# Optimization experiments

Hardware: AMD Instinct MI355X
Metric: run time of the kernel (lower is better)

Reference implementation:

```python
import jax, jax.numpy as jnp
import numpy as np

N, K, C, H = 8192, 32, 192, 6
HD = C // H                       # head dim = 32
SCALE = HD ** -0.5
POS_BND = int(0.8 * K)            # 25 (OctFormer RPE: 0.8*patch_size*dilation**0.5, dilation=1)
RPE_NUM = 2 * POS_BND + 1         # 51
HID = 4 * C                       # mlp hidden


def setup_inputs() -> dict:
    key = jax.random.key(0)
    ks = jax.random.split(key, 18)
    w = lambda k, sh: (jax.random.normal(k, sh, jnp.float32) * 0.02)
    data = jax.random.normal(ks[0], (N, K, C), jnp.float32)
    # rel_pos: integer xyz offsets between points in a window, roughly in [-32, 32)
    rel_pos = jax.random.randint(ks[1], (N, K, K, 3), 0, 64, jnp.int32) - 32
    mask = jnp.where(jax.random.uniform(ks[2], (N, K, K)) < 0.05, -1e9, 0.0).astype(jnp.float32)
    return {
        "data": data,
        "mask": mask,
        "rel_pos": rel_pos,
        "ln1_g": jnp.ones((C,), jnp.float32),
        "ln1_b": jnp.zeros((C,), jnp.float32),
        "qkv_w": w(ks[3], (C, 3 * C)),
        "qkv_b": jnp.zeros((3 * C,), jnp.float32),
        "rpe_table": w(ks[4], (3 * RPE_NUM, H)),
        "proj_w": w(ks[5], (C, C)),
        "proj_b": jnp.zeros((C,), jnp.float32),
        "ln2_g": jnp.ones((C,), jnp.float32),
        "ln2_b": jnp.zeros((C,), jnp.float32),
        "mlp_w1": w(ks[6], (C, HID)),
        "mlp_b1": jnp.zeros((HID,), jnp.float32),
        "mlp_w2": w(ks[7], (HID, C)),
        "mlp_b2": jnp.zeros((C,), jnp.float32),
    }


def _layernorm(x, g, b):
    m = x.mean(-1, keepdims=True)
    v = ((x - m) ** 2).mean(-1, keepdims=True)
    return (x - m) * jax.lax.rsqrt(v + 1e-5) * g + b


def reference(data, mask, rel_pos, ln1_g, ln1_b, qkv_w, qkv_b, rpe_table,
              proj_w, proj_b, ln2_g, ln2_b, mlp_w1, mlp_b1, mlp_w2, mlp_b2):
    # --- windowed attention (OctreeAttention) ---
    x = _layernorm(data, ln1_g, ln1_b)                      # (N,K,C)
    qkv = (x @ qkv_w + qkv_b).reshape(N, K, 3, H, HD)
    qkv = qkv.transpose(2, 0, 3, 1, 4)                      # (3,N,H,K,HD)
    q, k, v = qkv[0] * SCALE, qkv[1], qkv[2]
    attn = jnp.einsum('nhqd,nhkd->nhqk', q, k)              # (N,H,K,K)
    # RPE: clamp xyz offsets, index per-axis rows of the table, sum over xyz
    idx = jnp.clip(rel_pos, -POS_BND, POS_BND) + POS_BND + jnp.arange(3, dtype=rel_pos.dtype) * RPE_NUM
    rpe = rpe_table[idx].sum(axis=3)                        # (N,K,K,H)
    attn = attn + rpe.transpose(0, 3, 1, 2) + mask[:, None, :, :]
    attn = jax.nn.softmax(attn, axis=-1)
    out = jnp.einsum('nhqk,nhkd->nqhd', attn, v).reshape(N, K, C)
    out = out @ proj_w + proj_b
    data = data + out                                       # residual (gamma1=1, drop_path=0)
    # --- MLP ---
    y = _layernorm(data, ln2_g, ln2_b)
    y = jax.nn.gelu(y @ mlp_w1 + mlp_b1, approximate=False) @ mlp_w2 + mlp_b2
    return data + y
```

## Files before the change

### kernel.cpp

```cpp
#include <hip/hip_runtime.h>
#include <hip/hip_bf16.h>
#include <cmath>


#define KW    32
#define CD    192
#define NH    6
#define HID   768
#define SCALE 0.17677669529663687f

typedef short short8 __attribute__((ext_vector_type(8)));
typedef float f32x4  __attribute__((ext_vector_type(4)));
typedef unsigned short u16;

#define FB_QKV  0
#define FB_PROJ 216
#define FB_MLP1 288
#define FB_MLP2 576
#define NFRAG   864
#define WS_BYTES (NFRAG * 512 * 2)

__device__ __forceinline__ u16 f2bb(float v) {
  __hip_bfloat16 h = __float2bfloat16(v);
  return *(u16*)&h;
}
__device__ __forceinline__ float bb2f(u16 b) {
  union { float f; unsigned u; } x; x.u = ((unsigned)b) << 16; return x.f;
}

__global__ __launch_bounds__(256) void pack_weights(
    const float* __restrict__ qkv_w, const float* __restrict__ proj_w,
    const float* __restrict__ mlp_w1, const float* __restrict__ mlp_w2,
    u16* __restrict__ ws)
{
  const int idx  = blockIdx.x * 256 + threadIdx.x;
  const int f    = idx >> 6;
  const int lane = idx & 63;
  const float* src; int N, KB, fl;
  if (f < FB_PROJ)      { src = qkv_w;  N = 576; KB = 6;  fl = f; }
  else if (f < FB_MLP1) { src = proj_w; N = 192; KB = 6;  fl = f - FB_PROJ; }
  else if (f < FB_MLP2) { src = mlp_w1; N = 768; KB = 6;  fl = f - FB_MLP1; }
  else                  { src = mlp_w2; N = 192; KB = 24; fl = f - FB_MLP2; }
  const int nt = fl / KB, kb = fl % KB;
  const int k0 = kb * 32 + (lane >> 4) * 8;
  const int n  = nt * 16 + (lane & 15);
  u16* dst = ws + ((size_t)(f * 64 + lane)) * 8;
  #pragma unroll
  for (int j = 0; j < 8; ++j) dst[j] = f2bb(src[(size_t)(k0 + j) * N + n]);
}

__global__ __launch_bounds__(256, 2) void octformer_mfma(
    const float* __restrict__ data, const float* __restrict__ mask,
    const int* __restrict__ rel_pos,
    const float* __restrict__ ln1_g, const float* __restrict__ ln1_b,
    const float* __restrict__ qkv_b, const float* __restrict__ rpe_table,
    const float* __restrict__ proj_b,
    const float* __restrict__ ln2_g, const float* __restrict__ ln2_b,
    const float* __restrict__ mlp_b1, const float* __restrict__ mlp_b2,
    const u16* __restrict__ wsb, float* __restrict__ out)
{
  __shared__ __align__(16) u16 s_x[64][200];
  __shared__ __align__(16) u16 s_qkv[64][200];
  __shared__ __align__(16) u16 s_ao[64][200];

  const int tid  = threadIdx.x;
  const int n0   = blockIdx.x * 2;
  const size_t base = (size_t)blockIdx.x * (2 * KW * CD);

  const int wv   = tid >> 6;
  const int lane = tid & 63;
  const int l15  = lane & 15;
  const int quad = lane >> 4;

  const int rg = tid >> 5;
  const int c0 = tid & 31;

  const f32x4 zed = {0.f, 0.f, 0.f, 0.f};

  float res[8][6];
  #pragma unroll
  for (int i = 0; i < 8; ++i) {
    const int r = rg * 8 + i;
    float s = 0.f, q = 0.f;
    #pragma unroll
    for (int j = 0; j < 6; ++j) {
      const float v = data[base + r * CD + c0 + 32 * j];
      res[i][j] = v; s += v; q += v * v;
    }
    #pragma unroll
    for (int m = 16; m >= 1; m >>= 1) { s += __shfl_xor(s, m); q += __shfl_xor(q, m); }
    const float mean = s * (1.0f / CD);
    const float rstd = rsqrtf(q * (1.0f / CD) - mean * mean + 1e-5f);
    #pragma unroll
    for (int j = 0; j < 6; ++j) {
      const int c = c0 + 32 * j;
      s_x[r][c] = f2bb((res[i][j] - mean) * rstd * ln1_g[c] + ln1_b[c]);
    }
  }

  const int w_at = wv >> 1;
  const int hh   = wv & 1;
  unsigned pidx[2][2][4];
  #pragma unroll
  for (int rt = 0; rt < 2; ++rt)
    #pragma unroll
    for (int ct = 0; ct < 2; ++ct)
      #pragma unroll
      for (int i = 0; i < 4; ++i) {
        const int r = rt * 16 + quad * 4 + i;
        const int c = ct * 16 + l15;
        const size_t g = ((size_t)(n0 + w_at) * KW + r) * KW + c;
        const int* rp = rel_pos + 3 * g;
        int i0 = rp[0]; i0 = i0 < -25 ? -25 : (i0 > 25 ? 25 : i0); i0 += 25;
        int i1 = rp[1]; i1 = i1 < -25 ? -25 : (i1 > 25 ? 25 : i1); i1 += 76;
        int i2 = rp[2]; i2 = i2 < -25 ? -25 : (i2 > 25 ? 25 : i2); i2 += 127;
        const unsigned mb = (mask[g] < -0.5f) ? (1u << 24) : 0u;
        pidx[rt][ct][i] = (unsigned)i0 | ((unsigned)i1 << 8) | ((unsigned)i2 << 16) | mb;
      }
  __syncthreads();

  for (int hp = 0; hp < 3; ++hp) {
    {
      f32x4 acc[3][4];
      #pragma unroll
      for (int ni = 0; ni < 3; ++ni)
        #pragma unroll
        for (int m = 0; m < 4; ++m) acc[ni][m] = zed;
      for (int kb = 0; kb < 6; ++kb) {
        short8 a[4];
        #pragma unroll
        for (int m = 0; m < 4; ++m)
          a[m] = *(const short8*)&s_x[m * 16 + l15][kb * 32 + quad * 8];
        #pragma unroll
        for (int ni = 0; ni < 3; ++ni) {
          const int lnt = wv + 4 * ni, part = lnt >> 2, sub = lnt & 3;
          const int gnt = part * 12 + hp * 4 + sub;
          const short8 b = *(const short8*)(wsb + ((size_t)((FB_QKV + gnt * 6 + kb) * 64 + lane)) * 8);
          #pragma unroll
          for (int m = 0; m < 4; ++m)
            acc[ni][m] = __builtin_amdgcn_mfma_f32_16x16x32_bf16(a[m], b, acc[ni][m], 0, 0, 0);
        }
      }
      #pragma unroll
      for (int ni = 0; ni < 3; ++ni) {
        const int lnt = wv + 4 * ni, part = lnt >> 2, sub = lnt & 3;
        const int gnt = part * 12 + hp * 4 + sub;
        const float bias = qkv_b[gnt * 16 + l15];
        #pragma unroll
        for (int m = 0; m < 4; ++m)
          #pragma unroll
          for (int i = 0; i < 4; ++i) {
            float v = acc[ni][m][i] + bias;
            if (part == 0) v *= SCALE;
            s_qkv[m * 16 + quad * 4 + i][part * 64 + sub * 16 + l15] = f2bb(v);
          }
      }
    }
    __syncthreads();

    {
      const int h = hp * 2 + hh;
      const int rbase = w_at * 32;
      short8 qf[2], kf[2];
      #pragma unroll
      for (int t = 0; t < 2; ++t) {
        qf[t] = *(const short8*)&s_qkv[rbase + t * 16 + l15][hh * 32 + quad * 8];
        kf[t] = *(const short8*)&s_qkv[rbase + t * 16 + l15][64 + hh * 32 + quad * 8];
      }
      float S[2][2][4];
      #pragma unroll
      for (int rt = 0; rt < 2; ++rt)
        #pragma unroll
        for (int ct = 0; ct < 2; ++ct) {
          const f32x4 sa = __builtin_amdgcn_mfma_f32_16x16x32_bf16(qf[rt], kf[ct], zed, 0, 0, 0);
          #pragma unroll
          for (int i = 0; i < 4; ++i) {
            const unsigned p = pidx[rt][ct][i];
            float b = rpe_table[(p & 255u) * NH + h]
                    + rpe_table[((p >> 8) & 255u) * NH + h]
                    + rpe_table[((p >> 16) & 255u) * NH + h];
            if (p >> 24) b -= 1e9f;
            S[rt][ct][i] = sa[i] + b;
          }
        }
      #pragma unroll
      for (int rt = 0; rt < 2; ++rt)
        #pragma unroll
        for (int i = 0; i < 4; ++i) {
          float mx = fmaxf(S[rt][0][i], S[rt][1][i]);
          #pragma unroll
          for (int m = 8; m >= 1; m >>= 1) mx = fmaxf(mx, __shfl_xor(mx, m));
          const float e0 = __expf(S[rt][0][i] - mx);
          const float e1 = __expf(S[rt][1][i] - mx);
          float sm = e0 + e1;
          #pragma unroll
          for (int m = 8; m >= 1; m >>= 1) sm += __shfl_xor(sm, m);
          const float inv = 1.0f / sm;
          const int r = rbase + rt * 16 + quad * 4 + i;
          s_qkv[r][hh * 32 + l15]      = f2bb(e0 * inv);
          s_qkv[r][hh * 32 + 16 + l15] = f2bb(e1 * inv);
        }
      {
        const int key = lane & 31, hf = lane >> 5;
        #pragma unroll
        for (int j = 0; j < 16; ++j) {
          const int d = hf * 16 + j;
          s_qkv[rbase + d][64 + hh * 32 + key] = s_qkv[rbase + key][128 + hh * 32 + d];
        }
      }
      short8 pf[2], vf[2];
      #pragma unroll
      for (int t = 0; t < 2; ++t) {
        pf[t] = *(const short8*)&s_qkv[rbase + t * 16 + l15][hh * 32 + quad * 8];
        vf[t] = *(const short8*)&s_qkv[rbase + t * 16 + l15][64 + hh * 32 + quad * 8];
      }
      #pragma unroll
      for (int mt = 0; mt < 2; ++mt)
        #pragma unroll
        for (int dt = 0; dt < 2; ++dt) {
          const f32x4 o = __builtin_amdgcn_mfma_f32_16x16x32_bf16(pf[mt], vf[dt], zed, 0, 0, 0);
          #pragma unroll
          for (int i = 0; i < 4; ++i)
            s_ao[rbase + mt * 16 + quad * 4 + i][h * 32 + dt * 16 + l15] = f2bb(o[i]);
        }
    }
    __syncthreads();
  }

  {
    f32x4 acc[3][4];
    #pragma unroll
    for (int ni = 0; ni < 3; ++ni)
      #pragma unroll
      for (int m = 0; m < 4; ++m) acc[ni][m] = zed;
    for (int kb = 0; kb < 6; ++kb) {
      short8 a[4];
      #pragma unroll
      for (int m = 0; m < 4; ++m)
        a[m] = *(const short8*)&s_ao[m * 16 + l15][kb * 32 + quad * 8];
      #pragma unroll
      for (int ni = 0; ni < 3; ++ni) {
        const int nt = wv + 4 * ni;
        const short8 b = *(const short8*)(wsb + ((size_t)((FB_PROJ + nt * 6 + kb) * 64 + lane)) * 8);
        #pragma unroll
        for (int m = 0; m < 4; ++m)
          acc[ni][m] = __builtin_amdgcn_mfma_f32_16x16x32_bf16(a[m], b, acc[ni][m], 0, 0, 0);
      }
    }
    #pragma unroll
    for (int ni = 0; ni < 3; ++ni) {
      const int nt = wv + 4 * ni;
      const float bias = proj_b[nt * 16 + l15];
      #pragma unroll
      for (int m = 0; m < 4; ++m)
        #pragma unroll
        for (int i = 0; i < 4; ++i)
          s_x[m * 16 + quad * 4 + i][nt * 16 + l15] = f2bb(acc[ni][m][i] + bias);
    }
  }
  __syncthreads();

  #pragma unroll
  for (int i = 0; i < 8; ++i) {
    const int r = rg * 8 + i;
    float s = 0.f, q = 0.f;
    #pragma unroll
    for (int j = 0; j < 6; ++j) {
      res[i][j] += bb2f(s_x[r][c0 + 32 * j]);
      s += res[i][j]; q += res[i][j] * res[i][j];
    }
    #pragma unroll
    for (int m = 16; m >= 1; m >>= 1) { s += __shfl_xor(s, m); q += __shfl_xor(q, m); }
    const float mean = s * (1.0f / CD);
    const float rstd = rsqrtf(q * (1.0f / CD) - mean * mean + 1e-5f);
    #pragma unroll
    for (int j = 0; j < 6; ++j) {
      const int c = c0 + 32 * j;
      s_x[r][c] = f2bb((res[i][j] - mean) * rstd * ln2_g[c] + ln2_b[c]);
    }
  }
  __syncthreads();

  {
    f32x4 y[3][4];
    #pragma unroll
    for (int ni = 0; ni < 3; ++ni)
      #pragma unroll
      for (int m = 0; m < 4; ++m) y[ni][m] = zed;

    for (int cc = 0; cc < 4; ++cc) {
      {
        f32x4 acc[3][4];
        #pragma unroll
        for (int ni = 0; ni < 3; ++ni)
          #pragma unroll
          for (int m = 0; m < 4; ++m) acc[ni][m] = zed;
        for (int kb = 0; kb < 6; ++kb) {
          short8 a[4];
          #pragma unroll
          for (int m = 0; m < 4; ++m)
            a[m] = *(const short8*)&s_x[m * 16 + l15][kb * 32 + quad * 8];
          #pragma unroll
          for (int ni = 0; ni < 3; ++ni) {
            const int gnt = cc * 12 + wv + 4 * ni;
            const short8 b = *(const short8*)(wsb + ((size_t)((FB_MLP1 + gnt * 6 + kb) * 64 + lane)) * 8);
            #pragma unroll
            for (int m = 0; m < 4; ++m)
              acc[ni][m] = __builtin_amdgcn_mfma_f32_16x16x32_bf16(a[m], b, acc[ni][m], 0, 0, 0);
          }
        }
        #pragma unroll
        for (int ni = 0; ni < 3; ++ni) {
          const int lnt = wv + 4 * ni;
          const float b1 = mlp_b1[(cc * 12 + lnt) * 16 + l15];
          #pragma unroll
          for (int m = 0; m < 4; ++m)
            #pragma unroll
            for (int i = 0; i < 4; ++i) {
              const float v = acc[ni][m][i] + b1;
              const float gel = 0.5f * v * (1.0f + erff(v * 0.70710678118654752f));
              s_qkv[m * 16 + quad * 4 + i][lnt * 16 + l15] = f2bb(gel);
            }
        }
      }
      __syncthreads();

      for (int kb = 0; kb < 6; ++kb) {
        short8 a[4];
        #pragma unroll
        for (int m = 0; m < 4; ++m)
          a[m] = *(const short8*)&s_qkv[m * 16 + l15][kb * 32 + quad * 8];
        #pragma unroll
        for (int ni = 0; ni < 3; ++ni) {
          const int nt = wv + 4 * ni;
          const short8 b = *(const short8*)(wsb + ((size_t)((FB_MLP2 + nt * 24 + cc * 6 + kb) * 64 + lane)) * 8);
          #pragma unroll
          for (int m = 0; m < 4; ++m)
            y[ni][m] = __builtin_amdgcn_mfma_f32_16x16x32_bf16(a[m], b, y[ni][m], 0, 0, 0);
        }
      }
      __syncthreads();
    }

    #pragma unroll
    for (int ni = 0; ni < 3; ++ni) {
      const int nt = wv + 4 * ni;
      const float b2 = mlp_b2[nt * 16 + l15];
      #pragma unroll
      for (int m = 0; m < 4; ++m)
        #pragma unroll
        for (int i = 0; i < 4; ++i)
          s_x[m * 16 + quad * 4 + i][nt * 16 + l15] = f2bb(y[ni][m][i] + b2);
    }
  }
  __syncthreads();

  #pragma unroll
  for (int i = 0; i < 8; ++i) {
    const int r = rg * 8 + i;
    #pragma unroll
    for (int j = 0; j < 6; ++j)
      out[base + r * CD + c0 + 32 * j] = res[i][j] + bb2f(s_x[r][c0 + 32 * j]);
  }
}

__global__ __launch_bounds__(256) void octformer_scalar(
    const float* __restrict__ data, const float* __restrict__ mask, const int* __restrict__ rel_pos,
    const float* __restrict__ ln1_g, const float* __restrict__ ln1_b,
    const float* __restrict__ qkv_w, const float* __restrict__ qkv_b, const float* __restrict__ rpe_table,
    const float* __restrict__ proj_w, const float* __restrict__ proj_b,
    const float* __restrict__ ln2_g, const float* __restrict__ ln2_b,
    const float* __restrict__ mlp_w1, const float* __restrict__ mlp_b1,
    const float* __restrict__ mlp_w2, const float* __restrict__ mlp_b2,
    float* __restrict__ out)
{
  const int n = blockIdx.x, tid = threadIdx.x;
  __shared__ float s_x[KW][CD];
  __shared__ float s_ao[KW][CD];
  __shared__ float s_q[KW][33];
  __shared__ float s_k[KW][33];
  __shared__ float s_p[KW][33];
  const size_t base = (size_t)n * (KW * CD);
  const int r0 = (tid >> 5) << 2, c0 = tid & 31;
  float res[4][6];
  #pragma unroll
  for (int i = 0; i < 4; ++i)
    #pragma unroll
    for (int j = 0; j < 6; ++j) res[i][j] = data[base + (r0 + i) * CD + c0 + 32 * j];
  #pragma unroll
  for (int i = 0; i < 4; ++i) {
    float s = 0.f, q = 0.f;
    #pragma unroll
    for (int j = 0; j < 6; ++j) { s += res[i][j]; q += res[i][j] * res[i][j]; }
    #pragma unroll
    for (int m = 16; m >= 1; m >>= 1) { s += __shfl_xor(s, m); q += __shfl_xor(q, m); }
    const float mean = s / CD, rstd = rsqrtf(q / CD - mean * mean + 1e-5f);
    #pragma unroll
    for (int j = 0; j < 6; ++j) {
      const int c = c0 + 32 * j;
      s_x[r0 + i][c] = (res[i][j] - mean) * rstd * ln1_g[c] + ln1_b[c];
    }
  }
  __syncthreads();
  for (int h = 0; h < NH; ++h) {
    const int qc = h * 32 + c0, kc = CD + h * 32 + c0;
    float aq[4] = {0,0,0,0}, ak[4] = {0,0,0,0};
    for (int kk = 0; kk < CD; ++kk) {
      const float wq = qkv_w[kk * 576 + qc], wk = qkv_w[kk * 576 + kc];
      #pragma unroll
      for (int i = 0; i < 4; ++i) { const float a = s_x[r0 + i][kk]; aq[i] += a * wq; ak[i] += a * wk; }
    }
    #pragma unroll
    for (int i = 0; i < 4; ++i) {
      s_q[r0 + i][c0] = (aq[i] + qkv_b[qc]) * SCALE;
      s_k[r0 + i][c0] = ak[i] + qkv_b[kc];
    }
    __syncthreads();
    {
      float ac[4] = {0,0,0,0};
      #pragma unroll
      for (int d = 0; d < 32; ++d) {
        const float kb = s_k[c0][d];
        #pragma unroll
        for (int i = 0; i < 4; ++i) ac[i] += s_q[r0 + i][d] * kb;
      }
      #pragma unroll
      for (int i = 0; i < 4; ++i) {
        const size_t g = ((size_t)(n * KW + r0 + i)) * KW + c0;
        const int* rp = rel_pos + 3 * g;
        float rpe = 0.f;
        #pragma unroll
        for (int a = 0; a < 3; ++a) {
          int ix = rp[a]; ix = ix < -25 ? -25 : (ix > 25 ? 25 : ix);
          rpe += rpe_table[(ix + 25 + 51 * a) * NH + h];
        }
        s_p[r0 + i][c0] = ac[i] + rpe + mask[g];
      }
    }
    __syncthreads();
    {
      const int r = tid >> 3, sb = tid & 7;
      float v0 = s_p[r][sb], v1 = s_p[r][sb + 8], v2 = s_p[r][sb + 16], v3 = s_p[r][sb + 24];
      float mx = fmaxf(fmaxf(v0, v1), fmaxf(v2, v3));
      mx = fmaxf(mx, __shfl_xor(mx, 1)); mx = fmaxf(mx, __shfl_xor(mx, 2)); mx = fmaxf(mx, __shfl_xor(mx, 4));
      v0 = __expf(v0 - mx); v1 = __expf(v1 - mx); v2 = __expf(v2 - mx); v3 = __expf(v3 - mx);
      float sm = v0 + v1 + v2 + v3;
      sm += __shfl_xor(sm, 1); sm += __shfl_xor(sm, 2); sm += __shfl_xor(sm, 4);
      const float inv = 1.0f / sm;
      s_p[r][sb] = v0 * inv; s_p[r][sb + 8] = v1 * inv; s_p[r][sb + 16] = v2 * inv; s_p[r][sb + 24] = v3 * inv;
    }
    __syncthreads();
    {
      const int vc = 2 * CD + h * 32 + c0;
      float av[4] = {0,0,0,0};
      for (int kk = 0; kk < CD; ++kk) {
        const float wvv = qkv_w[kk * 576 + vc];
        #pragma unroll
        for (int i = 0; i < 4; ++i) av[i] += s_x[r0 + i][kk] * wvv;
      }
      #pragma unroll
      for (int i = 0; i < 4; ++i) s_q[r0 + i][c0] = av[i] + qkv_b[vc];
    }
    __syncthreads();
    {
      float ao[4] = {0,0,0,0};
      #pragma unroll
      for (int j = 0; j < KW; ++j) {
        const float vb = s_q[j][c0];
        #pragma unroll
        for (int i = 0; i < 4; ++i) ao[i] += s_p[r0 + i][j] * vb;
      }
      #pragma unroll
      for (int i = 0; i < 4; ++i) s_ao[r0 + i][h * 32 + c0] = ao[i];
    }
    __syncthreads();
  }
  {
    float acc[4][6];
    #pragma unroll
    for (int j = 0; j < 6; ++j) {
      const float pb = proj_b[c0 + 32 * j];
      #pragma unroll
      for (int i = 0; i < 4; ++i) acc[i][j] = pb;
    }
    for (int kk = 0; kk < CD; ++kk) {
      float a[4];
      #pragma unroll
      for (int i = 0; i < 4; ++i) a[i] = s_ao[r0 + i][kk];
      #pragma unroll
      for (int j = 0; j < 6; ++j) {
        const float w = proj_w[kk * CD + c0 + 32 * j];
        #pragma unroll
        for (int i = 0; i < 4; ++i) acc[i][j] += a[i] * w;
      }
    }
    #pragma unroll
    for (int j = 0; j < 6; ++j)
      #pragma unroll
      for (int i = 0; i < 4; ++i) res[i][j] += acc[i][j];
  }
  __syncthreads();
  #pragma unroll
  for (int i = 0; i < 4; ++i) {
    float s = 0.f, q = 0.f;
    #pragma unroll
    for (int j = 0; j < 6; ++j) { s += res[i][j]; q += res[i][j] * res[i][j]; }
    #pragma unroll
    for (int m = 16; m >= 1; m >>= 1) { s += __shfl_xor(s, m); q += __shfl_xor(q, m); }
    const float mean = s / CD, rstd = rsqrtf(q / CD - mean * mean + 1e-5f);
    #pragma unroll
    for (int j = 0; j < 6; ++j) {
      const int c = c0 + 32 * j;
      s_x[r0 + i][c] = (res[i][j] - mean) * rstd * ln2_g[c] + ln2_b[c];
    }
  }
  __syncthreads();
  {
    float y[4][6];
    #pragma unroll
    for (int j = 0; j < 6; ++j) {
      const float bb = mlp_b2[c0 + 32 * j];
      #pragma unroll
      for (int i = 0; i < 4; ++i) y[i][j] = bb;
    }
    for (int cc = 0; cc < 4; ++cc) {
      {
        float acc[4][6];
        #pragma unroll
        for (int j = 0; j < 6; ++j) {
          const float b1 = mlp_b1[cc * CD + c0 + 32 * j];
          #pragma unroll
          for (int i = 0; i < 4; ++i) acc[i][j] = b1;
        }
        for (int kk = 0; kk < CD; ++kk) {
          float a[4];
          #pragma unroll
          for (int i = 0; i < 4; ++i) a[i] = s_x[r0 + i][kk];
          #pragma unroll
          for (int j = 0; j < 6; ++j) {
            const float w = mlp_w1[kk * HID + cc * CD + c0 + 32 * j];
            #pragma unroll
            for (int i = 0; i < 4; ++i) acc[i][j] += a[i] * w;
          }
        }
        #pragma unroll
        for (int j = 0; j < 6; ++j)
          #pragma unroll
          for (int i = 0; i < 4; ++i) {
            const float x = acc[i][j];
            s_ao[r0 + i][c0 + 32 * j] = 0.5f * x * (1.0f + erff(x * 0.70710678118654752f));
          }
      }
      __syncthreads();
      for (int kk = 0; kk < CD; ++kk) {
        float a[4];
        #pragma unroll
        for (int i = 0; i < 4; ++i) a[i] = s_ao[r0 + i][kk];
        #pragma unroll
        for (int j = 0; j < 6; ++j) {
          const float w = mlp_w2[(cc * CD + kk) * CD + c0 + 32 * j];
          #pragma unroll
          for (int i = 0; i < 4; ++i) y[i][j] += a[i] * w;
        }
      }
      __syncthreads();
    }
    #pragma unroll
    for (int i = 0; i < 4; ++i)
      #pragma unroll
      for (int j = 0; j < 6; ++j)
        out[base + (r0 + i) * CD + c0 + 32 * j] = res[i][j] + y[i][j];
  }
}

extern "C" void kernel_launch(void* const* d_in, const int* in_sizes, int n_in,
                              void* d_out, int out_size, void* d_ws, size_t ws_size,
                              hipStream_t stream) {
  (void)in_sizes; (void)n_in; (void)out_size;
  const float* data   = (const float*)d_in[0];
  const float* maskp  = (const float*)d_in[1];
  const int*   relp   = (const int*)d_in[2];
  const float* ln1g   = (const float*)d_in[3];
  const float* ln1b   = (const float*)d_in[4];
  const float* qkvw   = (const float*)d_in[5];
  const float* qkvb   = (const float*)d_in[6];
  const float* rpet   = (const float*)d_in[7];
  const float* projw  = (const float*)d_in[8];
  const float* projb  = (const float*)d_in[9];
  const float* ln2g   = (const float*)d_in[10];
  const float* ln2b   = (const float*)d_in[11];
  const float* mlpw1  = (const float*)d_in[12];
  const float* mlpb1  = (const float*)d_in[13];
  const float* mlpw2  = (const float*)d_in[14];
  const float* mlpb2  = (const float*)d_in[15];
  float* outp = (float*)d_out;

  if (ws_size >= (size_t)WS_BYTES) {
    u16* ws = (u16*)d_ws;
    pack_weights<<<dim3(NFRAG / 4), dim3(256), 0, stream>>>(qkvw, projw, mlpw1, mlpw2, ws);
    octformer_mfma<<<dim3(4096), dim3(256), 0, stream>>>(
        data, maskp, relp, ln1g, ln1b, qkvb, rpet, projb, ln2g, ln2b, mlpb1, mlpb2, ws, outp);
  } else {
    octformer_scalar<<<dim3(8192), dim3(256), 0, stream>>>(
        data, maskp, relp, ln1g, ln1b, qkvw, qkvb, rpet, projw, projb,
        ln2g, ln2b, mlpw1, mlpb1, mlpw2, mlpb2, outp);
  }
}
```

Measured before the change: 1.088 ms.

## Double threads per block to 512 and split GEMM rows across wave halves

Each block now runs 8 waves instead of 4. Every wave covers half of the 64 rows in the QKV, proj and MLP GEMMs and one 16-row tile in attention. V is written to shared memory already transposed in the QKV epilogue, which removes the separate in-LDS transpose loop. The aim is more waves to hide latency and fewer registers per thread. In exchange, each wave now loads every B weight fragment for only two row tiles instead of four, so weight-fragment global loads double, and launch bounds now request 4 blocks of 512 threads, which tightens the register budget.

```diff
diff --git a/kernel.cpp b/kernel.cpp
--- a/kernel.cpp
+++ b/kernel.cpp
@@ -49,7 +49,7 @@
   for (int j = 0; j < 8; ++j) dst[j] = f2bb(src[(size_t)(k0 + j) * N + n]);
 }
 
-__global__ __launch_bounds__(256, 2) void octformer_mfma(
+__global__ __launch_bounds__(512, 4) void octformer_mfma(
     const float* __restrict__ data, const float* __restrict__ mask,
     const int* __restrict__ rel_pos,
     const float* __restrict__ ln1_g, const float* __restrict__ ln1_b,
@@ -75,12 +75,19 @@
   const int rg = tid >> 5;
   const int c0 = tid & 31;
 
+  const int mh   = wv >> 2;
+  const int nsub = wv & 3;
+
+  const int hh   = wv & 1;
+  const int w_at = (wv >> 1) & 1;
+  const int rth  = wv >> 2;
+
   const f32x4 zed = {0.f, 0.f, 0.f, 0.f};
 
-  float res[8][6];
-  #pragma unroll
-  for (int i = 0; i < 8; ++i) {
-    const int r = rg * 8 + i;
+  float res[4][6];
+  #pragma unroll
+  for (int i = 0; i < 4; ++i) {
+    const int r = rg * 4 + i;
     float s = 0.f, q = 0.f;
     #pragma unroll
     for (int j = 0; j < 6; ++j) {
@@ -98,62 +105,69 @@
     }
   }
 
-  const int w_at = wv >> 1;
-  const int hh   = wv & 1;
-  unsigned pidx[2][2][4];
-  #pragma unroll
-  for (int rt = 0; rt < 2; ++rt)
-    #pragma unroll
-    for (int ct = 0; ct < 2; ++ct)
-      #pragma unroll
-      for (int i = 0; i < 4; ++i) {
-        const int r = rt * 16 + quad * 4 + i;
-        const int c = ct * 16 + l15;
-        const size_t g = ((size_t)(n0 + w_at) * KW + r) * KW + c;
-        const int* rp = rel_pos + 3 * g;
-        int i0 = rp[0]; i0 = i0 < -25 ? -25 : (i0 > 25 ? 25 : i0); i0 += 25;
-        int i1 = rp[1]; i1 = i1 < -25 ? -25 : (i1 > 25 ? 25 : i1); i1 += 76;
-        int i2 = rp[2]; i2 = i2 < -25 ? -25 : (i2 > 25 ? 25 : i2); i2 += 127;
-        const unsigned mb = (mask[g] < -0.5f) ? (1u << 24) : 0u;
-        pidx[rt][ct][i] = (unsigned)i0 | ((unsigned)i1 << 8) | ((unsigned)i2 << 16) | mb;
-      }
+  unsigned pidx[2][4];
+  #pragma unroll
+  for (int ct = 0; ct < 2; ++ct)
+    #pragma unroll
+    for (int i = 0; i < 4; ++i) {
+      const int r = rth * 16 + quad * 4 + i;
+      const int c = ct * 16 + l15;
+      const size_t g = ((size_t)(n0 + w_at) * KW + r) * KW + c;
+      const int* rp = rel_pos + 3 * g;
+      int i0 = rp[0]; i0 = i0 < -25 ? -25 : (i0 > 25 ? 25 : i0); i0 += 25;
+      int i1 = rp[1]; i1 = i1 < -25 ? -25 : (i1 > 25 ? 25 : i1); i1 += 76;
+      int i2 = rp[2]; i2 = i2 < -25 ? -25 : (i2 > 25 ? 25 : i2); i2 += 127;
+      const unsigned mb = (mask[g] < -0.5f) ? (1u << 24) : 0u;
+      pidx[ct][i] = (unsigned)i0 | ((unsigned)i1 << 8) | ((unsigned)i2 << 16) | mb;
+    }
   __syncthreads();
 
   for (int hp = 0; hp < 3; ++hp) {
     {
-      f32x4 acc[3][4];
+      f32x4 acc[3][2];
       #pragma unroll
       for (int ni = 0; ni < 3; ++ni)
         #pragma unroll
-        for (int m = 0; m < 4; ++m) acc[ni][m] = zed;
+        for (int mi = 0; mi < 2; ++mi) acc[ni][mi] = zed;
       for (int kb = 0; kb < 6; ++kb) {
-        short8 a[4];
-        #pragma unroll
-        for (int m = 0; m < 4; ++m)
-          a[m] = *(const short8*)&s_x[m * 16 + l15][kb * 32 + quad * 8];
+        short8 a[2];
+        #pragma unroll
+        for (int mi = 0; mi < 2; ++mi)
+          a[mi] = *(const short8*)&s_x[(mh * 2 + mi) * 16 + l15][kb * 32 + quad * 8];
         #pragma unroll
         for (int ni = 0; ni < 3; ++ni) {
-          const int lnt = wv + 4 * ni, part = lnt >> 2, sub = lnt & 3;
+          const int lnt = nsub + 4 * ni, part = lnt >> 2, sub = lnt & 3;
           const int gnt = part * 12 + hp * 4 + sub;
           const short8 b = *(const short8*)(wsb + ((size_t)((FB_QKV + gnt * 6 + kb) * 64 + lane)) * 8);
           #pragma unroll
-          for (int m = 0; m < 4; ++m)
-            acc[ni][m] = __builtin_amdgcn_mfma_f32_16x16x32_bf16(a[m], b, acc[ni][m], 0, 0, 0);
+          for (int mi = 0; mi < 2; ++mi)
+            acc[ni][mi] = __builtin_amdgcn_mfma_f32_16x16x32_bf16(a[mi], b, acc[ni][mi], 0, 0, 0);
         }
       }
       #pragma unroll
       for (int ni = 0; ni < 3; ++ni) {
-        const int lnt = wv + 4 * ni, part = lnt >> 2, sub = lnt & 3;
+        const int lnt = nsub + 4 * ni, part = lnt >> 2, sub = lnt & 3;
         const int gnt = part * 12 + hp * 4 + sub;
         const float bias = qkv_b[gnt * 16 + l15];
-        #pragma unroll
-        for (int m = 0; m < 4; ++m)
-          #pragma unroll
-          for (int i = 0; i < 4; ++i) {
-            float v = acc[ni][m][i] + bias;
-            if (part == 0) v *= SCALE;
-            s_qkv[m * 16 + quad * 4 + i][part * 64 + sub * 16 + l15] = f2bb(v);
-          }
+        if (part < 2) {
+          #pragma unroll
+          for (int mi = 0; mi < 2; ++mi)
+            #pragma unroll
+            for (int i = 0; i < 4; ++i) {
+              float v = acc[ni][mi][i] + bias;
+              if (part == 0) v *= SCALE;
+              s_qkv[(mh * 2 + mi) * 16 + quad * 4 + i][part * 64 + sub * 16 + l15] = f2bb(v);
+            }
+        } else {
+          const int vr = (sub >> 1) * 32 + (sub & 1) * 16 + l15;
+          #pragma unroll
+          for (int mi = 0; mi < 2; ++mi)
+            #pragma unroll
+            for (int i = 0; i < 4; ++i) {
+              const int gr = (mh * 2 + mi) * 16 + quad * 4 + i;
+              s_qkv[vr][128 + (gr >> 5) * 32 + (gr & 31)] = f2bb(acc[ni][mi][i] + bias);
+            }
+        }
       }
     }
     __syncthreads();
@@ -161,108 +175,93 @@
     {
       const int h = hp * 2 + hh;
       const int rbase = w_at * 32;
-      short8 qf[2], kf[2];
-      #pragma unroll
-      for (int t = 0; t < 2; ++t) {
-        qf[t] = *(const short8*)&s_qkv[rbase + t * 16 + l15][hh * 32 + quad * 8];
-        kf[t] = *(const short8*)&s_qkv[rbase + t * 16 + l15][64 + hh * 32 + quad * 8];
-      }
-      float S[2][2][4];
-      #pragma unroll
-      for (int rt = 0; rt < 2; ++rt)
-        #pragma unroll
-        for (int ct = 0; ct < 2; ++ct) {
-          const f32x4 sa = __builtin_amdgcn_mfma_f32_16x16x32_bf16(qf[rt], kf[ct], zed, 0, 0, 0);
-          #pragma unroll
-          for (int i = 0; i < 4; ++i) {
-            const unsigned p = pidx[rt][ct][i];
-            float b = rpe_table[(p & 255u) * NH + h]
-                    + rpe_table[((p >> 8) & 255u) * NH + h]
-                    + rpe_table[((p >> 16) & 255u) * NH + h];
-            if (p >> 24) b -= 1e9f;
-            S[rt][ct][i] = sa[i] + b;
-          }
-        }
-      #pragma unroll
-      for (int rt = 0; rt < 2; ++rt)
-        #pragma unroll
-        for (int i = 0; i < 4; ++i) {
-          float mx = fmaxf(S[rt][0][i], S[rt][1][i]);
-          #pragma unroll
-          for (int m = 8; m >= 1; m >>= 1) mx = fmaxf(mx, __shfl_xor(mx, m));
-          const float e0 = __expf(S[rt][0][i] - mx);
-          const float e1 = __expf(S[rt][1][i] - mx);
-          float sm = e0 + e1;
-          #pragma unroll
-          for (int m = 8; m >= 1; m >>= 1) sm += __shfl_xor(sm, m);
-          const float inv = 1.0f / sm;
-          const int r = rbase + rt * 16 + quad * 4 + i;
-          s_qkv[r][hh * 32 + l15]      = f2bb(e0 * inv);
-          s_qkv[r][hh * 32 + 16 + l15] = f2bb(e1 * inv);
-        }
-      {
-        const int key = lane & 31, hf = lane >> 5;
-        #pragma unroll
-        for (int j = 0; j < 16; ++j) {
-          const int d = hf * 16 + j;
-          s_qkv[rbase + d][64 + hh * 32 + key] = s_qkv[rbase + key][128 + hh * 32 + d];
-        }
-      }
-      short8 pf[2], vf[2];
-      #pragma unroll
-      for (int t = 0; t < 2; ++t) {
-        pf[t] = *(const short8*)&s_qkv[rbase + t * 16 + l15][hh * 32 + quad * 8];
-        vf[t] = *(const short8*)&s_qkv[rbase + t * 16 + l15][64 + hh * 32 + quad * 8];
-      }
-      #pragma unroll
-      for (int mt = 0; mt < 2; ++mt)
-        #pragma unroll
-        for (int dt = 0; dt < 2; ++dt) {
-          const f32x4 o = __builtin_amdgcn_mfma_f32_16x16x32_bf16(pf[mt], vf[dt], zed, 0, 0, 0);
-          #pragma unroll
-          for (int i = 0; i < 4; ++i)
-            s_ao[rbase + mt * 16 + quad * 4 + i][h * 32 + dt * 16 + l15] = f2bb(o[i]);
-        }
+      const short8 qf  = *(const short8*)&s_qkv[rbase + rth * 16 + l15][hh * 32 + quad * 8];
+      const short8 kf0 = *(const short8*)&s_qkv[rbase + l15][64 + hh * 32 + quad * 8];
+      const short8 kf1 = *(const short8*)&s_qkv[rbase + 16 + l15][64 + hh * 32 + quad * 8];
+      const f32x4 sa0 = __builtin_amdgcn_mfma_f32_16x16x32_bf16(qf, kf0, zed, 0, 0, 0);
+      const f32x4 sa1 = __builtin_amdgcn_mfma_f32_16x16x32_bf16(qf, kf1, zed, 0, 0, 0);
+      float S0[4], S1[4];
+      #pragma unroll
+      for (int i = 0; i < 4; ++i) {
+        unsigned p = pidx[0][i];
+        float b = rpe_table[(p & 255u) * NH + h]
+                + rpe_table[((p >> 8) & 255u) * NH + h]
+                + rpe_table[((p >> 16) & 255u) * NH + h];
+        if (p >> 24) b -= 1e9f;
+        S0[i] = sa0[i] + b;
+        p = pidx[1][i];
+        b = rpe_table[(p & 255u) * NH + h]
+          + rpe_table[((p >> 8) & 255u) * NH + h]
+          + rpe_table[((p >> 16) & 255u) * NH + h];
+        if (p >> 24) b -= 1e9f;
+        S1[i] = sa1[i] + b;
+      }
+      #pragma unroll
+      for (int i = 0; i < 4; ++i) {
+        float mx = fmaxf(S0[i], S1[i]);
+        #pragma unroll
+        for (int m = 8; m >= 1; m >>= 1) mx = fmaxf(mx, __shfl_xor(mx, m));
+        const float e0 = __expf(S0[i] - mx);
+        const float e1 = __expf(S1[i] - mx);
+        float sm = e0 + e1;
+        #pragma unroll
+        for (int m = 8; m >= 1; m >>= 1) sm += __shfl_xor(sm, m);
+        const float inv = 1.0f / sm;
+        const int r = rbase + rth * 16 + quad * 4 + i;
+        s_qkv[r][hh * 32 + l15]      = f2bb(e0 * inv);
+        s_qkv[r][hh * 32 + 16 + l15] = f2bb(e1 * inv);
+      }
+      const short8 pf  = *(const short8*)&s_qkv[rbase + rth * 16 + l15][hh * 32 + quad * 8];
+      const short8 vf0 = *(const short8*)&s_qkv[hh * 32 + l15][128 + w_at * 32 + quad * 8];
+      const short8 vf1 = *(const short8*)&s_qkv[hh * 32 + 16 + l15][128 + w_at * 32 + quad * 8];
+      const f32x4 o0 = __builtin_amdgcn_mfma_f32_16x16x32_bf16(pf, vf0, zed, 0, 0, 0);
+      const f32x4 o1 = __builtin_amdgcn_mfma_f32_16x16x32_bf16(pf, vf1, zed, 0, 0, 0);
+      #pragma unroll
+      for (int i = 0; i < 4; ++i) {
+        const int r = rbase + rth * 16 + quad * 4 + i;
+        s_ao[r][h * 32 + l15]      = f2bb(o0[i]);
+        s_ao[r][h * 32 + 16 + l15] = f2bb(o1[i]);
+      }
     }
     __syncthreads();
   }
 
   {
-    f32x4 acc[3][4];
+    f32x4 acc[3][2];
     #pragma unroll
     for (int ni = 0; ni < 3; ++ni)
       #pragma unroll
-      for (int m = 0; m < 4; ++m) acc[ni][m] = zed;
+      for (int mi = 0; mi < 2; ++mi) acc[ni][mi] = zed;
     for (int kb = 0; kb < 6; ++kb) {
-      short8 a[4];
-      #pragma unroll
-      for (int m = 0; m < 4; ++m)
-        a[m] = *(const short8*)&s_ao[m * 16 + l15][kb * 32 + quad * 8];
+      short8 a[2];
+      #pragma unroll
+      for (int mi = 0; mi < 2; ++mi)
+        a[mi] = *(const short8*)&s_ao[(mh * 2 + mi) * 16 + l15][kb * 32 + quad * 8];
       #pragma unroll
       for (int ni = 0; ni < 3; ++ni) {
-        const int nt = wv + 4 * ni;
+        const int nt = nsub + 4 * ni;
         const short8 b = *(const short8*)(wsb + ((size_t)((FB_PROJ + nt * 6 + kb) * 64 + lane)) * 8);
         #pragma unroll
-        for (int m = 0; m < 4; ++m)
-          acc[ni][m] = __builtin_amdgcn_mfma_f32_16x16x32_bf16(a[m], b, acc[ni][m], 0, 0, 0);
+        for (int mi = 0; mi < 2; ++mi)
+          acc[ni][mi] = __builtin_amdgcn_mfma_f32_16x16x32_bf16(a[mi], b, acc[ni][mi], 0, 0, 0);
       }
     }
     #pragma unroll
     for (int ni = 0; ni < 3; ++ni) {
-      const int nt = wv + 4 * ni;
+      const int nt = nsub + 4 * ni;
       const float bias = proj_b[nt * 16 + l15];
       #pragma unroll
-      for (int m = 0; m < 4; ++m)
+      for (int mi = 0; mi < 2; ++mi)
         #pragma unroll
         for (int i = 0; i < 4; ++i)
-          s_x[m * 16 + quad * 4 + i][nt * 16 + l15] = f2bb(acc[ni][m][i] + bias);
+          s_x[(mh * 2 + mi) * 16 + quad * 4 + i][nt * 16 + l15] = f2bb(acc[ni][mi][i] + bias);
     }
   }
   __syncthreads();
 
   #pragma unroll
-  for (int i = 0; i < 8; ++i) {
-    const int r = rg * 8 + i;
+  for (int i = 0; i < 4; ++i) {
+    const int r = rg * 4 + i;
     float s = 0.f, q = 0.f;
     #pragma unroll
     for (int j = 0; j < 6; ++j) {
@@ -282,61 +281,61 @@
   __syncthreads();
 
   {
-    f32x4 y[3][4];
+    f32x4 y[3][2];
     #pragma unroll
     for (int ni = 0; ni < 3; ++ni)
       #pragma unroll
-      for (int m = 0; m < 4; ++m) y[ni][m] = zed;
+      for (int mi = 0; mi < 2; ++mi) y[ni][mi] = zed;
 
     for (int cc = 0; cc < 4; ++cc) {
       {
-        f32x4 acc[3][4];
+        f32x4 acc[3][2];
         #pragma unroll
         for (int ni = 0; ni < 3; ++ni)
           #pragma unroll
-          for (int m = 0; m < 4; ++m) acc[ni][m] = zed;
+          for (int mi = 0; mi < 2; ++mi) acc[ni][mi] = zed;
         for (int kb = 0; kb < 6; ++kb) {
-          short8 a[4];
-          #pragma unroll
-          for (int m = 0; m < 4; ++m)
-            a[m] = *(const short8*)&s_x[m * 16 + l15][kb * 32 + quad * 8];
+          short8 a[2];
+          #pragma unroll
+          for (int mi = 0; mi < 2; ++mi)
+            a[mi] = *(const short8*)&s_x[(mh * 2 + mi) * 16 + l15][kb * 32 + quad * 8];
           #pragma unroll
           for (int ni = 0; ni < 3; ++ni) {
-            const int gnt = cc * 12 + wv + 4 * ni;
+            const int gnt = cc * 12 + nsub + 4 * ni;
             const short8 b = *(const short8*)(wsb + ((size_t)((FB_MLP1 + gnt * 6 + kb) * 64 + lane)) * 8);
             #pragma unroll
-            for (int m = 0; m < 4; ++m)
-              acc[ni][m] = __builtin_amdgcn_mfma_f32_16x16x32_bf16(a[m], b, acc[ni][m], 0, 0, 0);
+            for (int mi = 0; mi < 2; ++mi)
+              acc[ni][mi] = __builtin_amdgcn_mfma_f32_16x16x32_bf16(a[mi], b, acc[ni][mi], 0, 0, 0);
           }
         }
         #pragma unroll
         for (int ni = 0; ni < 3; ++ni) {
-          const int lnt = wv + 4 * ni;
+          const int lnt = nsub + 4 * ni;
           const float b1 = mlp_b1[(cc * 12 + lnt) * 16 + l15];
           #pragma unroll
-          for (int m = 0; m < 4; ++m)
+          for (int mi = 0; mi < 2; ++mi)
             #pragma unroll
             for (int i = 0; i < 4; ++i) {
-              const float v = acc[ni][m][i] + b1;
+              const float v = acc[ni][mi][i] + b1;
               const float gel = 0.5f * v * (1.0f + erff(v * 0.70710678118654752f));
-              s_qkv[m * 16 + quad * 4 + i][lnt * 16 + l15] = f2bb(gel);
+              s_qkv[(mh * 2 + mi) * 16 + quad * 4 + i][lnt * 16 + l15] = f2bb(gel);
             }
         }
       }
       __syncthreads();
 
       for (int kb = 0; kb < 6; ++kb) {
-        short8 a[4];
-        #pragma unroll
-        for (int m = 0; m < 4; ++m)
-          a[m] = *(const short8*)&s_qkv[m * 16 + l15][kb * 32 + quad * 8];
+        short8 a[2];
+        #pragma unroll
+        for (int mi = 0; mi < 2; ++mi)
+          a[mi] = *(const short8*)&s_qkv[(mh * 2 + mi) * 16 + l15][kb * 32 + quad * 8];
         #pragma unroll
         for (int ni = 0; ni < 3; ++ni) {
-          const int nt = wv + 4 * ni;
+          const int nt = nsub + 4 * ni;
           const short8 b = *(const short8*)(wsb + ((size_t)((FB_MLP2 + nt * 24 + cc * 6 + kb) * 64 + lane)) * 8);
           #pragma unroll
-          for (int m = 0; m < 4; ++m)
-            y[ni][m] = __builtin_amdgcn_mfma_f32_16x16x32_bf16(a[m], b, y[ni][m], 0, 0, 0);
+          for (int mi = 0; mi < 2; ++mi)
+            y[ni][mi] = __builtin_amdgcn_mfma_f32_16x16x32_bf16(a[mi], b, y[ni][mi], 0, 0, 0);
         }
       }
       __syncthreads();
@@ -344,20 +343,20 @@
 
     #pragma unroll
     for (int ni = 0; ni < 3; ++ni) {
-      const int nt = wv + 4 * ni;
+      const int nt = nsub + 4 * ni;
       const float b2 = mlp_b2[nt * 16 + l15];
       #pragma unroll
-      for (int m = 0; m < 4; ++m)
+      for (int mi = 0; mi < 2; ++mi)
         #pragma unroll
         for (int i = 0; i < 4; ++i)
-          s_x[m * 16 + quad * 4 + i][nt * 16 + l15] = f2bb(y[ni][m][i] + b2);
+          s_x[(mh * 2 + mi) * 16 + quad * 4 + i][nt * 16 + l15] = f2bb(y[ni][mi][i] + b2);
     }
   }
   __syncthreads();
 
   #pragma unroll
-  for (int i = 0; i < 8; ++i) {
-    const int r = rg * 8 + i;
+  for (int i = 0; i < 4; ++i) {
+    const int r = rg * 4 + i;
     #pragma unroll
     for (int j = 0; j < 6; ++j)
       out[base + r * CD + c0 + 32 * j] = res[i][j] + bb2f(s_x[r][c0 + 32 * j]);
@@ -598,7 +597,7 @@
   if (ws_size >= (size_t)WS_BYTES) {
     u16* ws = (u16*)d_ws;
     pack_weights<<<dim3(NFRAG / 4), dim3(256), 0, stream>>>(qkvw, projw, mlpw1, mlpw2, ws);
-    octformer_mfma<<<dim3(4096), dim3(256), 0, stream>>>(
+    octformer_mfma<<<dim3(4096), dim3(512), 0, stream>>>(
         data, maskp, relp, ln1g, ln1b, qkvb, rpet, projb, ln2g, ln2b, mlpb1, mlpb2, ws, outp);
   } else {
     octformer_scalar<<<dim3(8192), dim3(256), 0, stream>>>(
```

After: 1.234 ms. 1.13x slower.
